# Optimization experiments

Hardware: AMD Instinct MI355X
Metric: run time of the kernel (lower is better)

The kernel has to match this reference:

```python
import jax, jax.numpy as jnp
import numpy as np

N = 100000      # nodes
E = 1600000     # directed edges (avg degree 16)
F_IN = 512      # config.input_layer
H1, D1 = 8, 8   # conv1: 8 heads x 8 dims
C_OUT = 40      # config.output_layer


def setup_inputs() -> dict:
    key = jax.random.key(0)
    ks = jax.random.split(key, 10)
    x = jax.random.normal(ks[0], (N, F_IN), dtype=jnp.float32)
    edge_index = jax.random.randint(ks[1], (2, E), 0, N, dtype=jnp.int64)
    s = 0.05
    W1 = jax.random.normal(ks[2], (F_IN, H1 * D1), dtype=jnp.float32) * s
    att_src1 = jax.random.normal(ks[3], (H1, D1), dtype=jnp.float32) * s
    att_dst1 = jax.random.normal(ks[4], (H1, D1), dtype=jnp.float32) * s
    b1 = jnp.zeros((H1 * D1,), dtype=jnp.float32)
    W2 = jax.random.normal(ks[5], (H1 * D1, C_OUT), dtype=jnp.float32) * s
    att_src2 = jax.random.normal(ks[6], (1, C_OUT), dtype=jnp.float32) * s
    att_dst2 = jax.random.normal(ks[7], (1, C_OUT), dtype=jnp.float32) * s
    b2 = jnp.zeros((C_OUT,), dtype=jnp.float32)
    return {"x": x, "edge_index": edge_index,
            "W1": W1, "att_src1": att_src1, "att_dst1": att_dst1, "b1": b1,
            "W2": W2, "att_src2": att_src2, "att_dst2": att_dst2, "b2": b2}


def _gat_conv(x, src, dst, W, a_src, a_dst, b, heads, concat):
    """PyG GATConv (eval mode: attention dropout is identity)."""
    n = x.shape[0]
    d = W.shape[1] // heads
    h = (x @ W).reshape(n, heads, d)                       # [N,H,D]
    alpha_s = jnp.einsum('nhd,hd->nh', h, a_src)           # [N,H]
    alpha_d = jnp.einsum('nhd,hd->nh', h, a_dst)
    e = jax.nn.leaky_relu(alpha_s[src] + alpha_d[dst], 0.2)  # [E,H]
    # numerically stable segment softmax over edges grouped by dst
    e = e - jax.ops.segment_max(e, dst, num_segments=n)[dst]
    ex = jnp.exp(e)
    denom = jax.ops.segment_sum(ex, dst, num_segments=n)[dst]
    alpha = ex / denom                                      # [E,H]
    msg = h[src] * alpha[:, :, None]                        # [E,H,D]
    out = jax.ops.segment_sum(msg, dst, num_segments=n)     # [N,H,D]
    out = out.reshape(n, heads * d) if concat else out.mean(axis=1)
    return out + b


def reference(x, edge_index, W1, att_src1, att_dst1, b1, W2, att_src2, att_dst2, b2):
    # add self loops (PyG GATConv default)
    loop = jnp.arange(x.shape[0], dtype=edge_index.dtype)
    src = jnp.concatenate([edge_index[0], loop])
    dst = jnp.concatenate([edge_index[1], loop])
    # dropout(p=0.6) layers are identity in eval mode
    h = jax.nn.elu(_gat_conv(x, src, dst, W1, att_src1, att_dst1, b1, H1, True))
    out = _gat_conv(h, src, dst, W2, att_src2, att_dst2, b2, 1, False)
    return jax.nn.log_softmax(out, axis=1)
```

## Files before the change

kernel.cpp:

```cpp
#include <hip/hip_runtime.h>

#define F_IN 512
#define H1   8
#define D1   8
#define C1   64
#define C2   40

#define BKT_SH   7
#define BKT_W    128
#define NBKT_MAX 1024
#define NBLK     128

using short8 = __attribute__((ext_vector_type(8))) short;
using f32x4  = __attribute__((ext_vector_type(4))) float;
using bf8v   = __attribute__((ext_vector_type(8))) __bf16;

__device__ __forceinline__ float leaky02(float x) { return x > 0.f ? x : 0.2f * x; }

__device__ __forceinline__ short8 cvt_bf16x8(float4 a, float4 b) {
    bf8v r;
    r[0] = (__bf16)a.x; r[1] = (__bf16)a.y; r[2] = (__bf16)a.z; r[3] = (__bf16)a.w;
    r[4] = (__bf16)b.x; r[5] = (__bf16)b.y; r[6] = (__bf16)b.z; r[7] = (__bf16)b.w;
    return __builtin_bit_cast(short8, r);
}

__global__ __launch_bounds__(256) void wconv_kernel(
    const float* __restrict__ W1, unsigned short* __restrict__ Btg)
{
    int idx = blockIdx.x * 256 + threadIdx.x;
    if (idx >= F_IN * C1) return;
    int k = idx >> 6, c = idx & 63;
    unsigned u = __builtin_bit_cast(unsigned, W1[idx]);
    unsigned short h = (unsigned short)((u + 0x7FFFu + ((u >> 16) & 1u)) >> 16);
    Btg[(size_t)c * F_IN + k] = h;
}

__global__ __launch_bounds__(256) void gemm1_kernel(
    const float* __restrict__ x, const unsigned short* __restrict__ Btg,
    float* __restrict__ h1, int N)
{
    const int tid  = threadIdx.x;
    const int w    = tid >> 6;
    const int lane = tid & 63;
    const int lo   = lane & 15;
    const int kg   = lane >> 4;
    const int n0   = blockIdx.x * 128 + w * 32;

    const int nA = min(n0 + lo, N - 1);
    const int nB = min(n0 + 16 + lo, N - 1);
    const float* xA = x + (size_t)nA * F_IN + kg * 8;
    const float* xB = x + (size_t)nB * F_IN + kg * 8;
    const unsigned short* bp = Btg + (size_t)lo * F_IN + kg * 8;

    f32x4 acc[2][4];
    #pragma unroll
    for (int mt = 0; mt < 2; ++mt)
        #pragma unroll
        for (int nt = 0; nt < 4; ++nt)
            acc[mt][nt] = (f32x4){0.f, 0.f, 0.f, 0.f};

    #pragma unroll 4
    for (int s = 0; s < 16; ++s) {
        const int kb = s * 32;
        float4 a0 = *(const float4*)(xA + kb);
        float4 a1 = *(const float4*)(xA + kb + 4);
        float4 c0 = *(const float4*)(xB + kb);
        float4 c1 = *(const float4*)(xB + kb + 4);
        short8 bF[4];
        #pragma unroll
        for (int nt = 0; nt < 4; ++nt)
            bF[nt] = *(const short8*)(bp + (size_t)nt * 16 * F_IN + kb);
        short8 aF0 = cvt_bf16x8(a0, a1);
        short8 aF1 = cvt_bf16x8(c0, c1);
        #pragma unroll
        for (int nt = 0; nt < 4; ++nt) {
            acc[0][nt] = __builtin_amdgcn_mfma_f32_16x16x32_bf16(aF0, bF[nt], acc[0][nt], 0, 0, 0);
            acc[1][nt] = __builtin_amdgcn_mfma_f32_16x16x32_bf16(aF1, bF[nt], acc[1][nt], 0, 0, 0);
        }
    }

    #pragma unroll
    for (int mt = 0; mt < 2; ++mt) {
        #pragma unroll
        for (int j = 0; j < 4; ++j) {
            const int n = n0 + mt * 16 + kg * 4 + j;
            if (n < N) {
                #pragma unroll
                for (int nt = 0; nt < 4; ++nt)
                    h1[(size_t)n * C1 + nt * 16 + lo] = acc[mt][nt][j];
            }
        }
    }
}

__global__ __launch_bounds__(256) void alpha1_kernel(
    const float* __restrict__ h1, const float* __restrict__ a_src,
    const float* __restrict__ a_dst, float* __restrict__ as1,
    float* __restrict__ ad1, int N)
{
    const int n = blockIdx.x * 4 + (threadIdx.x >> 6);
    if (n >= N) return;
    const int lane = threadIdx.x & 63;
    float v  = h1[(size_t)n * C1 + lane];
    float ps = v * a_src[lane], pd = v * a_dst[lane];
    ps += __shfl_xor(ps, 1); pd += __shfl_xor(pd, 1);
    ps += __shfl_xor(ps, 2); pd += __shfl_xor(pd, 2);
    ps += __shfl_xor(ps, 4); pd += __shfl_xor(pd, 4);
    if (!(lane & 7)) {
        as1[n * H1 + (lane >> 3)] = ps;
        ad1[n * H1 + (lane >> 3)] = pd;
    }
}

__global__ __launch_bounds__(256) void bhist_kernel(
    const int* __restrict__ ei, int* __restrict__ blockhist,
    int E, int nbkt, int chunk)
{
    __shared__ int lh[NBKT_MAX];
    for (int i = threadIdx.x; i < nbkt; i += 256) lh[i] = 0;
    __syncthreads();
    const int b = blockIdx.x;
    const int beg = b * chunk;
    const int end = min(E, beg + chunk);
    for (int e = beg + threadIdx.x; e < end; e += 256)
        atomicAdd(&lh[ei[E + e] >> BKT_SH], 1);
    __syncthreads();
    for (int k = threadIdx.x; k < nbkt; k += 256)
        blockhist[k * NBLK + b] = lh[k];
}

__global__ __launch_bounds__(512) void scan1_kernel(
    const int* __restrict__ in, int* __restrict__ excl,
    int* __restrict__ bsum, int M)
{
    __shared__ int sA[512], sB[512];
    const int t = threadIdx.x;
    const int i = blockIdx.x * 512 + t;
    int v = (i < M) ? in[i] : 0;
    sA[t] = v; __syncthreads();
    int* pin = sA; int* pout = sB;
    #pragma unroll
    for (int off = 1; off < 512; off <<= 1) {
        pout[t] = pin[t] + ((t >= off) ? pin[t - off] : 0);
        __syncthreads();
        int* tmp = pin; pin = pout; pout = tmp;
    }
    if (i < M) excl[i] = pin[t] - v;
    if (t == 511) bsum[blockIdx.x] = pin[511];
}

__global__ __launch_bounds__(256) void scan2_kernel(
    int* __restrict__ bsum, int* __restrict__ bsumo, int NB)
{
    __shared__ int sA[256], sB[256];
    const int t = threadIdx.x;
    int v = (t < NB) ? bsum[t] : 0;
    sA[t] = v; __syncthreads();
    int* pin = sA; int* pout = sB;
    #pragma unroll
    for (int off = 1; off < 256; off <<= 1) {
        pout[t] = pin[t] + ((t >= off) ? pin[t - off] : 0);
        __syncthreads();
        int* tmp = pin; pin = pout; pout = tmp;
    }
    if (t < NB) bsumo[t] = pin[t] - v;
}

__global__ __launch_bounds__(512) void scan3_kernel(
    int* __restrict__ boffs, const int* __restrict__ bsumo, int M, int E)
{
    const int i = blockIdx.x * 512 + threadIdx.x;
    if (i < M) boffs[i] += bsumo[blockIdx.x];
    if (i == 0) boffs[M] = E;
}

__global__ __launch_bounds__(256) void bpart_kernel(
    const int* __restrict__ ei, const int* __restrict__ boffs,
    int2* __restrict__ ebuf, int E, int nbkt, int chunk)
{
    __shared__ int cur[NBKT_MAX];
    const int b = blockIdx.x;
    for (int k = threadIdx.x; k < nbkt; k += 256) cur[k] = boffs[k * NBLK + b];
    __syncthreads();
    const int beg = b * chunk;
    const int end = min(E, beg + chunk);
    for (int e = beg + threadIdx.x; e < end; e += 256) {
        int src = ei[e], dst = ei[E + e];
        int pos = atomicAdd(&cur[dst >> BKT_SH], 1);
        ebuf[pos] = make_int2(src, dst);
    }
}

__global__ __launch_bounds__(256) void bsort_kernel(
    const int* __restrict__ boffs, const int2* __restrict__ ebuf,
    int* __restrict__ rowptr, int* __restrict__ esrc, int N, int E)
{
    const int b = blockIdx.x;
    const int tid = threadIdx.x;
    const int base = boffs[b * NBLK];
    const int cnt  = boffs[(b + 1) * NBLK] - base;

    __shared__ int hist[BKT_W], scn[BKT_W], cur[BKT_W];
    if (tid < BKT_W) hist[tid] = 0;
    __syncthreads();
    for (int i = tid; i < cnt; i += 256)
        atomicAdd(&hist[ebuf[base + i].y & (BKT_W - 1)], 1);
    __syncthreads();
    if (tid < BKT_W) scn[tid] = hist[tid];
    __syncthreads();
    #pragma unroll
    for (int off = 1; off < BKT_W; off <<= 1) {
        int add = 0;
        if (tid < BKT_W && tid >= off) add = scn[tid - off];
        __syncthreads();
        if (tid < BKT_W) scn[tid] += add;
        __syncthreads();
    }
    if (tid < BKT_W) {
        int ex = base + scn[tid] - hist[tid];
        cur[tid] = ex;
        int n0 = b * BKT_W + tid;
        if (n0 < N) rowptr[n0] = ex;
    }
    if (b == 0 && tid == 0) rowptr[N] = E;
    __syncthreads();
    for (int i = tid; i < cnt; i += 256) {
        int2 ed = ebuf[base + i];
        int pos = atomicAdd(&cur[ed.y & (BKT_W - 1)], 1);
        esrc[pos] = ed.x;
    }
}

__global__ __launch_bounds__(256) void agg1_kernel(
    const int* __restrict__ rowptr, const int* __restrict__ esrc,
    const float* __restrict__ h1, const float* __restrict__ as1,
    const float* __restrict__ ad1, const float* __restrict__ b1,
    float* __restrict__ h1f, int N)
{
    const int n = blockIdx.x * 4 + (threadIdx.x >> 6);
    if (n >= N) return;
    const int lane = threadIdx.x & 63;
    const int h = lane >> 3;
    const float adh = ad1[n * H1 + h];

    float acc = 0.f, den = 0.f;
    int i = rowptr[n];
    const int end = rowptr[n + 1];
    for (; i + 4 <= end; i += 4) {
        const int s0 = esrc[i], s1 = esrc[i + 1], s2 = esrc[i + 2], s3 = esrc[i + 3];
        const float v0 = h1[(size_t)s0 * C1 + lane];
        const float v1 = h1[(size_t)s1 * C1 + lane];
        const float v2 = h1[(size_t)s2 * C1 + lane];
        const float v3 = h1[(size_t)s3 * C1 + lane];
        const float a0 = as1[s0 * H1 + h], a1 = as1[s1 * H1 + h];
        const float a2 = as1[s2 * H1 + h], a3 = as1[s3 * H1 + h];
        const float e0 = __expf(leaky02(a0 + adh));
        const float e1 = __expf(leaky02(a1 + adh));
        const float e2 = __expf(leaky02(a2 + adh));
        const float e3 = __expf(leaky02(a3 + adh));
        acc += e0 * v0; acc += e1 * v1; acc += e2 * v2; acc += e3 * v3;
        den += (e0 + e1) + (e2 + e3);
    }
    for (; i < end; ++i) {
        const int src = esrc[i];
        const float v  = h1[(size_t)src * C1 + lane];
        const float ex = __expf(leaky02(as1[src * H1 + h] + adh));
        acc += ex * v;
        den += ex;
    }
    {
        const float ex = __expf(leaky02(as1[n * H1 + h] + adh));
        acc += ex * h1[(size_t)n * C1 + lane];
        den += ex;
    }
    float v = acc / den + b1[lane];
    h1f[(size_t)n * C1 + lane] = v > 0.f ? v : __expf(v) - 1.f;
}

__global__ __launch_bounds__(320) void gemm2_kernel(
    const float* __restrict__ h1f, const float* __restrict__ W2,
    const float* __restrict__ a_src2, const float* __restrict__ a_dst2,
    float* __restrict__ h2, float* __restrict__ as2, float* __restrict__ ad2,
    int N)
{
    __shared__ float hs[8][C1];
    __shared__ float W2s[C1 * C2];
    __shared__ float redS[8][C2], redD[8][C2];
    const int tid = threadIdx.x;
    const int n0  = blockIdx.x * 8;
    for (int i = tid; i < 8 * C1; i += 320) hs[i >> 6][i & 63] = h1f[(size_t)n0 * C1 + i];
    for (int i = tid; i < C1 * C2; i += 320) W2s[i] = W2[i];
    __syncthreads();
    const int g = tid / C2, c = tid % C2;
    float acc = 0.f;
    #pragma unroll
    for (int k = 0; k < C1; ++k) acc += hs[g][k] * W2s[k * C2 + c];
    const int n = n0 + g;
    h2[(size_t)n * C2 + c] = acc;
    redS[g][c] = acc * a_src2[c];
    redD[g][c] = acc * a_dst2[c];
    __syncthreads();
    if (c == 0) {
        float s = 0.f, d = 0.f;
        for (int j = 0; j < C2; ++j) { s += redS[g][j]; d += redD[g][j]; }
        as2[n] = s; ad2[n] = d;
    }
}

__global__ __launch_bounds__(256) void agg2_kernel(
    const int* __restrict__ rowptr, const int* __restrict__ esrc,
    const float* __restrict__ h2, const float* __restrict__ as2,
    const float* __restrict__ ad2, const float* __restrict__ b2,
    float* __restrict__ out, int N)
{
    const int n = blockIdx.x * 4 + (threadIdx.x >> 6);
    if (n >= N) return;
    const int lane = threadIdx.x & 63;
    const float adn = ad2[n];

    float acc = 0.f, den = 0.f;
    int i = rowptr[n];
    const int end = rowptr[n + 1];
    for (; i + 4 <= end; i += 4) {
        const int s0 = esrc[i], s1 = esrc[i + 1], s2 = esrc[i + 2], s3 = esrc[i + 3];
        float v0 = 0.f, v1 = 0.f, v2 = 0.f, v3 = 0.f;
        if (lane < C2) {
            v0 = h2[(size_t)s0 * C2 + lane];
            v1 = h2[(size_t)s1 * C2 + lane];
            v2 = h2[(size_t)s2 * C2 + lane];
            v3 = h2[(size_t)s3 * C2 + lane];
        }
        const float a0 = as2[s0], a1 = as2[s1], a2 = as2[s2], a3 = as2[s3];
        const float e0 = __expf(leaky02(a0 + adn));
        const float e1 = __expf(leaky02(a1 + adn));
        const float e2 = __expf(leaky02(a2 + adn));
        const float e3 = __expf(leaky02(a3 + adn));
        acc += e0 * v0; acc += e1 * v1; acc += e2 * v2; acc += e3 * v3;
        den += (e0 + e1) + (e2 + e3);
    }
    for (; i < end; ++i) {
        const int src = esrc[i];
        float v = 0.f;
        if (lane < C2) v = h2[(size_t)src * C2 + lane];
        const float ex = __expf(leaky02(as2[src] + adn));
        acc += ex * v;
        den += ex;
    }
    {
        const float ex = __expf(leaky02(as2[n] + adn));
        if (lane < C2) acc += ex * h2[(size_t)n * C2 + lane];
        den += ex;
    }
    float v = (lane < C2) ? (acc / den + b2[lane]) : -1e30f;
    float m = v;
    #pragma unroll
    for (int s = 1; s < 64; s <<= 1) m = fmaxf(m, __shfl_xor(m, s));
    float e2x = (lane < C2) ? __expf(v - m) : 0.f;
    #pragma unroll
    for (int s = 1; s < 64; s <<= 1) e2x += __shfl_xor(e2x, s);
    float lse = __logf(e2x);
    if (lane < C2) out[(size_t)n * C2 + lane] = v - m - lse;
}

extern "C" void kernel_launch(void* const* d_in, const int* in_sizes, int n_in,
                              void* d_out, int out_size, void* d_ws, size_t ws_size,
                              hipStream_t stream)
{
    const float* x    = (const float*)d_in[0];
    const int*   ei   = (const int*)  d_in[1];
    const float* W1   = (const float*)d_in[2];
    const float* as1w = (const float*)d_in[3];
    const float* ad1w = (const float*)d_in[4];
    const float* b1   = (const float*)d_in[5];
    const float* W2   = (const float*)d_in[6];
    const float* as2w = (const float*)d_in[7];
    const float* ad2w = (const float*)d_in[8];
    const float* b2   = (const float*)d_in[9];

    const int N = in_sizes[0] / F_IN;
    const int E = in_sizes[1] / 2;
    const int nbkt = (N + BKT_W - 1) >> BKT_SH;
    const int M    = nbkt * NBLK;
    const int chunk = (E + NBLK - 1) / NBLK;

    char* base = (char*)d_ws;
    auto carve = [&](size_t bytes) -> void* {
        void* p = (void*)base;
        base += (bytes + 255) & ~(size_t)255;
        return p;
    };
    float* h1     = (float*)carve((size_t)N * C1 * 4);
    float* h1f    = (float*)carve((size_t)N * C1 * 4);
    float* as1    = (float*)carve((size_t)N * H1 * 4);
    float* ad1    = (float*)carve((size_t)N * H1 * 4);
    float* h2     = (float*)carve((size_t)N * C2 * 4);
    float* as2    = (float*)carve((size_t)N * 4);
    float* ad2    = (float*)carve((size_t)N * 4);
    int*   rowptr = (int*)carve((size_t)(N + 1) * 4);
    int*   esrc   = (int*)carve((size_t)E * 4);
    int*   boffs  = (int*)carve((size_t)(M + 1) * 4);
    int*   bsum   = (int*)carve(256 * 4);
    int*   bsumo  = (int*)carve(256 * 4);
    unsigned short* Btg = (unsigned short*)carve((size_t)F_IN * C1 * 2);

    int2* ebuf = (int2*)h2;

    const int NB = (M + 511) / 512;

    wconv_kernel<<<(F_IN * C1 + 255) / 256, 256, 0, stream>>>(W1, Btg);

    bhist_kernel<<<NBLK, 256, 0, stream>>>(ei, boffs, E, nbkt, chunk);
    scan1_kernel<<<NB, 512, 0, stream>>>(boffs, boffs, bsum, M);
    scan2_kernel<<<1, 256, 0, stream>>>(bsum, bsumo, NB);
    scan3_kernel<<<NB, 512, 0, stream>>>(boffs, bsumo, M, E);
    bpart_kernel<<<NBLK, 256, 0, stream>>>(ei, boffs, ebuf, E, nbkt, chunk);
    bsort_kernel<<<nbkt, 256, 0, stream>>>(boffs, ebuf, rowptr, esrc, N, E);

    gemm1_kernel<<<(N + 127) / 128, 256, 0, stream>>>(x, Btg, h1, N);
    alpha1_kernel<<<(N + 3) / 4, 256, 0, stream>>>(h1, as1w, ad1w, as1, ad1, N);
    agg1_kernel<<<(N + 3) / 4, 256, 0, stream>>>(rowptr, esrc, h1, as1, ad1, b1, h1f, N);
    gemm2_kernel<<<N / 8, 320, 0, stream>>>(h1f, W2, as2w, ad2w, h2, as2, ad2, N);
    agg2_kernel<<<(N + 3) / 4, 256, 0, stream>>>(rowptr, esrc, h2, as2, ad2, b2,
                                                 (float*)d_out, N);
}
```

Baseline: 384.4 us.

## Store node features in bf16, fuse alpha into GEMM1, MFMA for GEMM2

```diff
diff --git a/kernel.cpp b/kernel.cpp
--- a/kernel.cpp
+++ b/kernel.cpp
@@ -5,6 +5,7 @@
 #define D1   8
 #define C1   64
 #define C2   40
+#define C2P  48
 
 #define BKT_SH   7
 #define BKT_W    128
@@ -16,7 +17,12 @@
 using bf8v   = __attribute__((ext_vector_type(8))) __bf16;
 
 __device__ __forceinline__ float leaky02(float x) { return x > 0.f ? x : 0.2f * x; }
-
+__device__ __forceinline__ float bf2f(unsigned short u) {
+    return __builtin_bit_cast(float, ((unsigned)u) << 16);
+}
+__device__ __forceinline__ unsigned short f2bf(float v) {
+    return __builtin_bit_cast(unsigned short, (__bf16)v);
+}
 __device__ __forceinline__ short8 cvt_bf16x8(float4 a, float4 b) {
     bf8v r;
     r[0] = (__bf16)a.x; r[1] = (__bf16)a.y; r[2] = (__bf16)a.z; r[3] = (__bf16)a.w;
@@ -25,19 +31,26 @@
 }
 
 __global__ __launch_bounds__(256) void wconv_kernel(
-    const float* __restrict__ W1, unsigned short* __restrict__ Btg)
+    const float* __restrict__ W1, const float* __restrict__ W2,
+    unsigned short* __restrict__ Bt1, unsigned short* __restrict__ Bt2)
 {
     int idx = blockIdx.x * 256 + threadIdx.x;
-    if (idx >= F_IN * C1) return;
-    int k = idx >> 6, c = idx & 63;
-    unsigned u = __builtin_bit_cast(unsigned, W1[idx]);
-    unsigned short h = (unsigned short)((u + 0x7FFFu + ((u >> 16) & 1u)) >> 16);
-    Btg[(size_t)c * F_IN + k] = h;
+    if (idx < F_IN * C1) {
+        int k = idx >> 6, c = idx & 63;
+        Bt1[(size_t)c * F_IN + k] = f2bf(W1[idx]);
+    } else if (idx < F_IN * C1 + C2P * 64) {
+        int j = idx - F_IN * C1;
+        int c = j >> 6, k = j & 63;
+        float v = (c < C2) ? W2[k * C2 + c] : 0.f;
+        Bt2[c * 64 + k] = f2bf(v);
+    }
 }
 
 __global__ __launch_bounds__(256) void gemm1_kernel(
-    const float* __restrict__ x, const unsigned short* __restrict__ Btg,
-    float* __restrict__ h1, int N)
+    const float* __restrict__ x, const unsigned short* __restrict__ Bt1,
+    const float* __restrict__ a_src, const float* __restrict__ a_dst,
+    unsigned short* __restrict__ h1b, float* __restrict__ as1,
+    float* __restrict__ ad1, int N)
 {
     const int tid  = threadIdx.x;
     const int w    = tid >> 6;
@@ -50,7 +63,14 @@
     const int nB = min(n0 + 16 + lo, N - 1);
     const float* xA = x + (size_t)nA * F_IN + kg * 8;
     const float* xB = x + (size_t)nB * F_IN + kg * 8;
-    const unsigned short* bp = Btg + (size_t)lo * F_IN + kg * 8;
+    const unsigned short* bp = Bt1 + (size_t)lo * F_IN + kg * 8;
+
+    float a_s[4], a_d[4];
+    #pragma unroll
+    for (int nt = 0; nt < 4; ++nt) {
+        a_s[nt] = a_src[nt * 16 + lo];
+        a_d[nt] = a_dst[nt * 16 + lo];
+    }
 
     f32x4 acc[2][4];
     #pragma unroll
@@ -84,31 +104,35 @@
         #pragma unroll
         for (int j = 0; j < 4; ++j) {
             const int n = n0 + mt * 16 + kg * 4 + j;
+            float sv[4], dv[4];
+            #pragma unroll
+            for (int nt = 0; nt < 4; ++nt) {
+                float v = acc[mt][nt][j];
+                sv[nt] = v * a_s[nt];
+                dv[nt] = v * a_d[nt];
+            }
+            #pragma unroll
+            for (int m = 1; m < 8; m <<= 1) {
+                #pragma unroll
+                for (int nt = 0; nt < 4; ++nt) {
+                    sv[nt] += __shfl_xor(sv[nt], m);
+                    dv[nt] += __shfl_xor(dv[nt], m);
+                }
+            }
             if (n < N) {
                 #pragma unroll
                 for (int nt = 0; nt < 4; ++nt)
-                    h1[(size_t)n * C1 + nt * 16 + lo] = acc[mt][nt][j];
+                    h1b[(size_t)n * C1 + nt * 16 + lo] = f2bf(acc[mt][nt][j]);
+                if ((lane & 7) == 0) {
+                    const int h0 = (lane >> 3) & 1;
+                    #pragma unroll
+                    for (int nt = 0; nt < 4; ++nt) {
+                        as1[n * H1 + h0 + nt * 2] = sv[nt];
+                        ad1[n * H1 + h0 + nt * 2] = dv[nt];
+                    }
+                }
             }
         }
-    }
-}
-
-__global__ __launch_bounds__(256) void alpha1_kernel(
-    const float* __restrict__ h1, const float* __restrict__ a_src,
-    const float* __restrict__ a_dst, float* __restrict__ as1,
-    float* __restrict__ ad1, int N)
-{
-    const int n = blockIdx.x * 4 + (threadIdx.x >> 6);
-    if (n >= N) return;
-    const int lane = threadIdx.x & 63;
-    float v  = h1[(size_t)n * C1 + lane];
-    float ps = v * a_src[lane], pd = v * a_dst[lane];
-    ps += __shfl_xor(ps, 1); pd += __shfl_xor(pd, 1);
-    ps += __shfl_xor(ps, 2); pd += __shfl_xor(pd, 2);
-    ps += __shfl_xor(ps, 4); pd += __shfl_xor(pd, 4);
-    if (!(lane & 7)) {
-        as1[n * H1 + (lane >> 3)] = ps;
-        ad1[n * H1 + (lane >> 3)] = pd;
     }
 }
 
@@ -233,9 +257,9 @@
 
 __global__ __launch_bounds__(256) void agg1_kernel(
     const int* __restrict__ rowptr, const int* __restrict__ esrc,
-    const float* __restrict__ h1, const float* __restrict__ as1,
+    const unsigned short* __restrict__ h1b, const float* __restrict__ as1,
     const float* __restrict__ ad1, const float* __restrict__ b1,
-    float* __restrict__ h1f, int N)
+    unsigned short* __restrict__ h1f, int N)
 {
     const int n = blockIdx.x * 4 + (threadIdx.x >> 6);
     if (n >= N) return;
@@ -248,10 +272,10 @@
     const int end = rowptr[n + 1];
     for (; i + 4 <= end; i += 4) {
         const int s0 = esrc[i], s1 = esrc[i + 1], s2 = esrc[i + 2], s3 = esrc[i + 3];
-        const float v0 = h1[(size_t)s0 * C1 + lane];
-        const float v1 = h1[(size_t)s1 * C1 + lane];
-        const float v2 = h1[(size_t)s2 * C1 + lane];
-        const float v3 = h1[(size_t)s3 * C1 + lane];
+        const float v0 = bf2f(h1b[(size_t)s0 * C1 + lane]);
+        const float v1 = bf2f(h1b[(size_t)s1 * C1 + lane]);
+        const float v2 = bf2f(h1b[(size_t)s2 * C1 + lane]);
+        const float v3 = bf2f(h1b[(size_t)s3 * C1 + lane]);
         const float a0 = as1[s0 * H1 + h], a1 = as1[s1 * H1 + h];
         const float a2 = as1[s2 * H1 + h], a3 = as1[s3 * H1 + h];
         const float e0 = __expf(leaky02(a0 + adh));
@@ -263,53 +287,83 @@
     }
     for (; i < end; ++i) {
         const int src = esrc[i];
-        const float v  = h1[(size_t)src * C1 + lane];
+        const float v  = bf2f(h1b[(size_t)src * C1 + lane]);
         const float ex = __expf(leaky02(as1[src * H1 + h] + adh));
         acc += ex * v;
         den += ex;
     }
     {
         const float ex = __expf(leaky02(as1[n * H1 + h] + adh));
-        acc += ex * h1[(size_t)n * C1 + lane];
+        acc += ex * bf2f(h1b[(size_t)n * C1 + lane]);
         den += ex;
     }
     float v = acc / den + b1[lane];
-    h1f[(size_t)n * C1 + lane] = v > 0.f ? v : __expf(v) - 1.f;
-}
-
-__global__ __launch_bounds__(320) void gemm2_kernel(
-    const float* __restrict__ h1f, const float* __restrict__ W2,
+    v = v > 0.f ? v : __expf(v) - 1.f;
+    h1f[(size_t)n * C1 + lane] = f2bf(v);
+}
+
+__global__ __launch_bounds__(256) void gemm2_kernel(
+    const unsigned short* __restrict__ h1f, const unsigned short* __restrict__ Bt2,
     const float* __restrict__ a_src2, const float* __restrict__ a_dst2,
-    float* __restrict__ h2, float* __restrict__ as2, float* __restrict__ ad2,
-    int N)
-{
-    __shared__ float hs[8][C1];
-    __shared__ float W2s[C1 * C2];
-    __shared__ float redS[8][C2], redD[8][C2];
-    const int tid = threadIdx.x;
-    const int n0  = blockIdx.x * 8;
-    for (int i = tid; i < 8 * C1; i += 320) hs[i >> 6][i & 63] = h1f[(size_t)n0 * C1 + i];
-    for (int i = tid; i < C1 * C2; i += 320) W2s[i] = W2[i];
-    __syncthreads();
-    const int g = tid / C2, c = tid % C2;
-    float acc = 0.f;
-    #pragma unroll
-    for (int k = 0; k < C1; ++k) acc += hs[g][k] * W2s[k * C2 + c];
-    const int n = n0 + g;
-    h2[(size_t)n * C2 + c] = acc;
-    redS[g][c] = acc * a_src2[c];
-    redD[g][c] = acc * a_dst2[c];
-    __syncthreads();
-    if (c == 0) {
-        float s = 0.f, d = 0.f;
-        for (int j = 0; j < C2; ++j) { s += redS[g][j]; d += redD[g][j]; }
-        as2[n] = s; ad2[n] = d;
+    unsigned short* __restrict__ h2b, float* __restrict__ as2,
+    float* __restrict__ ad2, int N)
+{
+    const int tid  = threadIdx.x;
+    const int w    = tid >> 6;
+    const int lane = tid & 63;
+    const int lo   = lane & 15;
+    const int kg   = lane >> 4;
+    const int n0   = blockIdx.x * 64 + w * 16;
+
+    const int nA = min(n0 + lo, N - 1);
+    const unsigned short* ap = h1f + (size_t)nA * C1 + kg * 8;
+
+    float a_s[3], a_d[3];
+    #pragma unroll
+    for (int nt = 0; nt < 3; ++nt) {
+        const int c = nt * 16 + lo;
+        a_s[nt] = (c < C2) ? a_src2[c] : 0.f;
+        a_d[nt] = (c < C2) ? a_dst2[c] : 0.f;
+    }
+
+    f32x4 acc[3];
+    #pragma unroll
+    for (int nt = 0; nt < 3; ++nt) acc[nt] = (f32x4){0.f, 0.f, 0.f, 0.f};
+
+    #pragma unroll
+    for (int ks = 0; ks < 2; ++ks) {
+        short8 aF = *(const short8*)(ap + ks * 32);
+        #pragma unroll
+        for (int nt = 0; nt < 3; ++nt) {
+            short8 bF = *(const short8*)(Bt2 + (nt * 16 + lo) * 64 + ks * 32 + kg * 8);
+            acc[nt] = __builtin_amdgcn_mfma_f32_16x16x32_bf16(aF, bF, acc[nt], 0, 0, 0);
+        }
+    }
+
+    #pragma unroll
+    for (int j = 0; j < 4; ++j) {
+        const int n = n0 + kg * 4 + j;
+        float s = acc[0][j] * a_s[0] + acc[1][j] * a_s[1] + acc[2][j] * a_s[2];
+        float d = acc[0][j] * a_d[0] + acc[1][j] * a_d[1] + acc[2][j] * a_d[2];
+        #pragma unroll
+        for (int m = 1; m < 16; m <<= 1) {
+            s += __shfl_xor(s, m);
+            d += __shfl_xor(d, m);
+        }
+        if (n < N) {
+            #pragma unroll
+            for (int nt = 0; nt < 3; ++nt) {
+                const int c = nt * 16 + lo;
+                if (c < C2) h2b[(size_t)n * C2 + c] = f2bf(acc[nt][j]);
+            }
+            if (lo == 0) { as2[n] = s; ad2[n] = d; }
+        }
     }
 }
 
 __global__ __launch_bounds__(256) void agg2_kernel(
     const int* __restrict__ rowptr, const int* __restrict__ esrc,
-    const float* __restrict__ h2, const float* __restrict__ as2,
+    const unsigned short* __restrict__ h2b, const float* __restrict__ as2,
     const float* __restrict__ ad2, const float* __restrict__ b2,
     float* __restrict__ out, int N)
 {
@@ -325,10 +379,10 @@
         const int s0 = esrc[i], s1 = esrc[i + 1], s2 = esrc[i + 2], s3 = esrc[i + 3];
         float v0 = 0.f, v1 = 0.f, v2 = 0.f, v3 = 0.f;
         if (lane < C2) {
-            v0 = h2[(size_t)s0 * C2 + lane];
-            v1 = h2[(size_t)s1 * C2 + lane];
-            v2 = h2[(size_t)s2 * C2 + lane];
-            v3 = h2[(size_t)s3 * C2 + lane];
+            v0 = bf2f(h2b[(size_t)s0 * C2 + lane]);
+            v1 = bf2f(h2b[(size_t)s1 * C2 + lane]);
+            v2 = bf2f(h2b[(size_t)s2 * C2 + lane]);
+            v3 = bf2f(h2b[(size_t)s3 * C2 + lane]);
         }
         const float a0 = as2[s0], a1 = as2[s1], a2 = as2[s2], a3 = as2[s3];
         const float e0 = __expf(leaky02(a0 + adn));
@@ -340,15 +394,14 @@
     }
     for (; i < end; ++i) {
         const int src = esrc[i];
-        float v = 0.f;
-        if (lane < C2) v = h2[(size_t)src * C2 + lane];
+        float v = (lane < C2) ? bf2f(h2b[(size_t)src * C2 + lane]) : 0.f;
         const float ex = __expf(leaky02(as2[src] + adn));
         acc += ex * v;
         den += ex;
     }
     {
         const float ex = __expf(leaky02(as2[n] + adn));
-        if (lane < C2) acc += ex * h2[(size_t)n * C2 + lane];
+        if (lane < C2) acc += ex * bf2f(h2b[(size_t)n * C2 + lane]);
         den += ex;
     }
     float v = (lane < C2) ? (acc / den + b2[lane]) : -1e30f;
@@ -389,11 +442,11 @@
         base += (bytes + 255) & ~(size_t)255;
         return p;
     };
-    float* h1     = (float*)carve((size_t)N * C1 * 4);
-    float* h1f    = (float*)carve((size_t)N * C1 * 4);
+    unsigned short* h1b = (unsigned short*)carve((size_t)N * C1 * 2);
+    unsigned short* h1f = (unsigned short*)carve((size_t)N * C1 * 2);
     float* as1    = (float*)carve((size_t)N * H1 * 4);
     float* ad1    = (float*)carve((size_t)N * H1 * 4);
-    float* h2     = (float*)carve((size_t)N * C2 * 4);
+    unsigned short* h2b = (unsigned short*)carve((size_t)N * C2 * 2);
     float* as2    = (float*)carve((size_t)N * 4);
     float* ad2    = (float*)carve((size_t)N * 4);
     int*   rowptr = (int*)carve((size_t)(N + 1) * 4);
@@ -401,13 +454,14 @@
     int*   boffs  = (int*)carve((size_t)(M + 1) * 4);
     int*   bsum   = (int*)carve(256 * 4);
     int*   bsumo  = (int*)carve(256 * 4);
-    unsigned short* Btg = (unsigned short*)carve((size_t)F_IN * C1 * 2);
-
-    int2* ebuf = (int2*)h2;
+    unsigned short* Bt1 = (unsigned short*)carve((size_t)F_IN * C1 * 2);
+    unsigned short* Bt2 = (unsigned short*)carve((size_t)C2P * 64 * 2);
+
+    int2* ebuf = (int2*)h1f;
 
     const int NB = (M + 511) / 512;
 
-    wconv_kernel<<<(F_IN * C1 + 255) / 256, 256, 0, stream>>>(W1, Btg);
+    wconv_kernel<<<(F_IN * C1 + C2P * 64 + 255) / 256, 256, 0, stream>>>(W1, W2, Bt1, Bt2);
 
     bhist_kernel<<<NBLK, 256, 0, stream>>>(ei, boffs, E, nbkt, chunk);
     scan1_kernel<<<NB, 512, 0, stream>>>(boffs, boffs, bsum, M);
@@ -416,10 +470,9 @@
     bpart_kernel<<<NBLK, 256, 0, stream>>>(ei, boffs, ebuf, E, nbkt, chunk);
     bsort_kernel<<<nbkt, 256, 0, stream>>>(boffs, ebuf, rowptr, esrc, N, E);
 
-    gemm1_kernel<<<(N + 127) / 128, 256, 0, stream>>>(x, Btg, h1, N);
-    alpha1_kernel<<<(N + 3) / 4, 256, 0, stream>>>(h1, as1w, ad1w, as1, ad1, N);
-    agg1_kernel<<<(N + 3) / 4, 256, 0, stream>>>(rowptr, esrc, h1, as1, ad1, b1, h1f, N);
-    gemm2_kernel<<<N / 8, 320, 0, stream>>>(h1f, W2, as2w, ad2w, h2, as2, ad2, N);
-    agg2_kernel<<<(N + 3) / 4, 256, 0, stream>>>(rowptr, esrc, h2, as2, ad2, b2,
+    gemm1_kernel<<<(N + 127) / 128, 256, 0, stream>>>(x, Bt1, as1w, ad1w, h1b, as1, ad1, N);
+    agg1_kernel<<<(N + 3) / 4, 256, 0, stream>>>(rowptr, esrc, h1b, as1, ad1, b1, h1f, N);
+    gemm2_kernel<<<(N + 63) / 64, 256, 0, stream>>>(h1f, Bt2, as2w, ad2w, h2b, as2, ad2, N);
+    agg2_kernel<<<(N + 3) / 4, 256, 0, stream>>>(rowptr, esrc, h2b, as2, ad2, b2,
                                                  (float*)d_out, N);
 }
```

Measured after the change: 336.0 us. -12.6%, faster.
